# Optimization experiments

Measured on AMD Instinct MI355X. Metric: run time of the kernel, lower is better.

Reference implementation:

```python
import jax, jax.numpy as jnp
import numpy as np

D = 256                      # covariance dim, hardcoded by bottleneck Conv2d(_, 256, 1)
ITER_N = 5                   # SqrtmLayer(output, 5)
_r, _c = np.triu_indices(D)
FLAT_IDX = jnp.asarray(_r * D + _c)   # upper-tri (incl. diag) indices into flattened d*d


def setup_inputs() -> dict:
    key = jax.random.key(0)
    ks = jax.random.split(key, 5)
    B, C, H, W = 64, 2048, 16, 16
    num_classes = 4
    feats = D * (D + 1) // 2  # 32896
    return {
        "features": jax.random.normal(ks[0], (B, C, H, W), jnp.float32),
        "w_bn": jax.random.normal(ks[1], (D, C), jnp.float32) * 0.02,
        "b_bn": jnp.zeros((D,), jnp.float32),
        "w_type": jax.random.normal(ks[2], (num_classes, feats), jnp.float32) * 0.01,
        "b_type": jnp.zeros((num_classes,), jnp.float32),
        "w_flag": jax.random.normal(ks[3], (1, feats), jnp.float32) * 0.01,
        "b_flag": jnp.zeros((1,), jnp.float32),
    }


def _covpool(x):
    # x: [B, d, h, w] -> second-order pooling: x_f @ I_hat @ x_f^T, equivalent
    # to (1/M) * centered @ centered^T  (I_hat = -1/M^2 * ones + 1/M * eye)
    B, d, h, w = x.shape
    M = h * w
    xf = x.reshape(B, d, M)
    centered = xf - xf.mean(axis=2, keepdims=True)
    return jnp.einsum('bim,bjm->bij', centered, centered) / M  # [B, d, d]


def _sqrtm_ns(A, iter_n=ITER_N):
    # Newton-Schulz iteration for matrix square root (iSQRT-COV style)
    B, d, _ = A.shape
    I3 = 3.0 * jnp.eye(d, dtype=A.dtype)
    normA = jnp.trace(A, axis1=1, axis2=2)          # [B], pre-normalization
    An = A / normA[:, None, None]
    ZY = 0.5 * (I3 - An)
    Y = jnp.matmul(An, ZY)
    Z = ZY
    for _ in range(iter_n - 2):
        ZY = 0.5 * (I3 - jnp.matmul(Z, Y))
        Y = jnp.matmul(Y, ZY)
        Z = jnp.matmul(ZY, Z)
    YZY = 0.5 * jnp.matmul(Y, I3 - jnp.matmul(Z, Y))
    return YZY * jnp.sqrt(normA)[:, None, None]     # post-compensation


def reference(features, w_bn, b_bn, w_type, b_type, w_flag, b_flag):
    # 1x1 bottleneck conv: [B, C, H, W] -> [B, 256, H, W]
    x = jnp.einsum('bchw,oc->bohw', features, w_bn) + b_bn[None, :, None, None]
    cov = _covpool(x)                # [B, 256, 256]
    s = _sqrtm_ns(cov)               # [B, 256, 256]
    B = s.shape[0]
    vec = s.reshape(B, D * D)[:, FLAT_IDX]   # triu-vec: [B, 32896]
    type_logits = vec @ w_type.T + b_type    # [B, num_classes]
    flag_logits = vec @ w_flag.T + b_flag    # [B, 1]
    return (type_logits, flag_logits)
```

## Files before the change

kernel.cpp:

```cpp
#include <hip/hip_runtime.h>
#include <math.h>


typedef __attribute__((ext_vector_type(8))) short bf16x8;
typedef __attribute__((ext_vector_type(4))) float f32x4;
typedef __attribute__((ext_vector_type(4))) unsigned u32x4;
typedef __attribute__((ext_vector_type(2))) unsigned u32x2;

__device__ __forceinline__ unsigned fbits(float f) { union { float f; unsigned u; } x; x.f = f; return x.u; }
__device__ __forceinline__ float bitsf(unsigned u) { union { float f; unsigned u; } x; x.u = u; return x.f; }
__device__ __forceinline__ float bf16v(short h) { return bitsf(((unsigned)(unsigned short)h) << 16); }

__device__ __forceinline__ unsigned pack_h(float a, float b) {
  return (fbits(a) >> 16) | (fbits(b) & 0xFFFF0000u);
}
__device__ __forceinline__ unsigned pack_l(float a, float b) {
  float la = a - bitsf(fbits(a) & 0xFFFF0000u);
  float lb = b - bitsf(fbits(b) & 0xFFFF0000u);
  return (fbits(la) >> 16) | (fbits(lb) & 0xFFFF0000u);
}

__device__ __forceinline__ const bf16x8* fragp(const char* M, int kt, int row,
                                               int g, int pl) {
  return (const bf16x8*)(M + (size_t)kt * 32768 + (size_t)row * 128 +
                         ((((pl << 2) + g) ^ (row & 7)) << 4));
}
__device__ __forceinline__ const bf16x8* fragl(const char* L, int kt, int row,
                                               int g, int pl) {
  return (const bf16x8*)(L + kt * 8192 + row * 128 +
                         ((((pl << 2) + g) ^ (row & 7)) << 4));
}

__device__ __forceinline__ void write_quad_g(char* M, int row, int k0,
                                             const float* v) {
  char* rp = M + (size_t)(k0 >> 5) * 32768 + (size_t)row * 128;
  const int s = (k0 & 31) >> 3, bo = (k0 & 7) * 2;
  *(u32x2*)(rp + (((s) ^ (row & 7)) << 4) + bo) =
      (u32x2){pack_h(v[0], v[1]), pack_h(v[2], v[3])};
  *(u32x2*)(rp + (((s + 4) ^ (row & 7)) << 4) + bo) =
      (u32x2){pack_l(v[0], v[1]), pack_l(v[2], v[3])};
}
__device__ __forceinline__ void write_quad_l(char* L, int row, int k0,
                                             const float* v) {
  char* rp = L + (k0 >> 5) * 8192 + row * 128;
  const int s = (k0 & 31) >> 3, bo = (k0 & 7) * 2;
  *(u32x2*)(rp + (((s) ^ (row & 7)) << 4) + bo) =
      (u32x2){pack_h(v[0], v[1]), pack_h(v[2], v[3])};
  *(u32x2*)(rp + (((s + 4) ^ (row & 7)) << 4) + bo) =
      (u32x2){pack_l(v[0], v[1]), pack_l(v[2], v[3])};
}
__device__ __forceinline__ void read_quad_g(const char* M, int row, int k0,
                                            float* v) {
  const char* rp = M + (size_t)(k0 >> 5) * 32768 + (size_t)row * 128;
  const int s = (k0 & 31) >> 3, bo = (k0 & 7) * 2;
  const u32x2 hq = *(const u32x2*)(rp + (((s) ^ (row & 7)) << 4) + bo);
  const u32x2 lq = *(const u32x2*)(rp + (((s + 4) ^ (row & 7)) << 4) + bo);
  v[0] = bitsf(hq[0] << 16) + bitsf(lq[0] << 16);
  v[1] = bitsf(hq[0] & 0xFFFF0000u) + bitsf(lq[0] & 0xFFFF0000u);
  v[2] = bitsf(hq[1] << 16) + bitsf(lq[1] << 16);
  v[3] = bitsf(hq[1] & 0xFFFF0000u) + bitsf(lq[1] & 0xFFFF0000u);
}

#define MFMA3(c, aH, aL, bH, bL)                                            \
  c = __builtin_amdgcn_mfma_f32_16x16x32_bf16(aL, bH, c, 0, 0, 0);          \
  c = __builtin_amdgcn_mfma_f32_16x16x32_bf16(aH, bL, c, 0, 0, 0);          \
  c = __builtin_amdgcn_mfma_f32_16x16x32_bf16(aH, bH, c, 0, 0, 0);

#define LGKM_BAR() do { asm volatile("s_waitcnt lgkmcnt(0)" ::: "memory"); \
                        __builtin_amdgcn_s_barrier(); } while (0)

__global__ __launch_bounds__(256) void prep_k(
    const float* __restrict__ w_bn, const float* __restrict__ w_type,
    const float* __restrict__ w_flag, char* __restrict__ Wf,
    float* __restrict__ W2)
{
  const int bid = blockIdx.x;
  if (bid < 64) {
    const int kt = bid, r = threadIdx.x;
    const float* src = w_bn + (size_t)r * 2048 + kt * 32;
    char* rp = Wf + (size_t)kt * 32768 + (size_t)r * 128;
#pragma unroll
    for (int s = 0; s < 4; ++s) {
      float x[8];
#pragma unroll
      for (int e = 0; e < 8; ++e) x[e] = src[s * 8 + e];
      *(u32x4*)(rp + ((s ^ (r & 7)) << 4)) =
          (u32x4){pack_h(x[0], x[1]), pack_h(x[2], x[3]),
                  pack_h(x[4], x[5]), pack_h(x[6], x[7])};
      *(u32x4*)(rp + (((s + 4) ^ (r & 7)) << 4)) =
          (u32x4){pack_l(x[0], x[1]), pack_l(x[2], x[3]),
                  pack_l(x[4], x[5]), pack_l(x[6], x[7])};
    }
  } else {
    const int idx = bid - 64;
    const int v = idx >> 6, chunk = idx & 63;
    const float* src = (v < 4) ? (w_type + (size_t)v * 32896) : w_flag;
    const int e0 = chunk * 1024 + threadIdx.x * 4;
#pragma unroll
    for (int q = 0; q < 4; ++q) {
      const int e = e0 + q;
      const int i = e >> 8, j = e & 255;
      const int r = i < j ? i : j, c = i < j ? j : i;
      const int t = r * 256 - (r * (r - 1)) / 2 + (c - r);
      W2[(size_t)v * 65536 + e] = src[t] * (i == j ? 1.0f : 0.5f);
    }
  }
}

__global__ __launch_bounds__(512) void conv4_k(
    const char* __restrict__ Wf, const float* __restrict__ F,
    char* __restrict__ X, const float* __restrict__ bias)
{
  __shared__ __align__(16) float bf32[2][64 * 36];
  __shared__ __align__(16) char bfmt[2][8192];

  const int tid = threadIdx.x, lane = tid & 63, w = tid >> 6;
  const int wr = w >> 1, wc = w & 1, fr = lane & 15, g = lane >> 4;
  const int jb = blockIdx.x * 64, bz = blockIdx.y;
  const float* Fb = F + (size_t)bz * 524288;

  const int blc = tid >> 4, blpx = (tid & 15) * 4;
  const int pkpx = tid >> 3, pkq = tid & 3, pkpl = (tid >> 2) & 1;

  f32x4 acc[4][2] = {};
  bf16x8 pa0[4][2], pa1[4][2];
  float4 bl0, bl1;

  auto bload = [&](int t, float4& r) {
    r = *(const float4*)(Fb + ((size_t)t * 32 + blc) * 256 + jb + blpx);
  };
  auto bf32w = [&](int buf, const float4& r) {
    float* p = &bf32[buf][0];
    p[(blpx + 0) * 36 + blc] = r.x;
    p[(blpx + 1) * 36 + blc] = r.y;
    p[(blpx + 2) * 36 + blc] = r.z;
    p[(blpx + 3) * 36 + blc] = r.w;
  };
  auto aload = [&](int t, bf16x8 (*pa)[2]) {
#pragma unroll
    for (int m = 0; m < 4; ++m) {
      const int r = wr * 64 + m * 16 + fr;
#pragma unroll
      for (int pl = 0; pl < 2; ++pl) pa[m][pl] = *fragp(Wf, t, r, g, pl);
    }
  };
  auto pack = [&](int buf) {
    const float* p = &bf32[buf][pkpx * 36 + pkq * 8];
    const f32x4 a = *(const f32x4*)(p);
    const f32x4 b = *(const f32x4*)(p + 4);
    u32x4 outv;
    if (pkpl == 0)
      outv = (u32x4){pack_h(a[0], a[1]), pack_h(a[2], a[3]),
                     pack_h(b[0], b[1]), pack_h(b[2], b[3])};
    else
      outv = (u32x4){pack_l(a[0], a[1]), pack_l(a[2], a[3]),
                     pack_l(b[0], b[1]), pack_l(b[2], b[3])};
    const int slot = ((pkpl << 2) + pkq) ^ (pkpx & 7);
    *(u32x4*)(&bfmt[buf][pkpx * 128 + slot * 16]) = outv;
  };
  auto gemmstep = [&](int buf, bf16x8 (*pa)[2]) {
    bf16x8 bH[2], bL[2];
#pragma unroll
    for (int n = 0; n < 2; ++n) {
      const int r = wc * 32 + n * 16 + fr;
      const char* rp = &bfmt[buf][r * 128];
      bH[n] = *(const bf16x8*)(rp + ((g ^ (r & 7)) << 4));
      bL[n] = *(const bf16x8*)(rp + (((g + 4) ^ (r & 7)) << 4));
    }
#pragma unroll
    for (int m = 0; m < 4; ++m)
#pragma unroll
      for (int n = 0; n < 2; ++n) {
        f32x4 c = acc[m][n];
        MFMA3(c, pa[m][0], pa[m][1], bH[n], bL[n]);
        acc[m][n] = c;
      }
  };

  bload(0, bl0);
  bf32w(0, bl0);
  bload(1, bl1);
  aload(0, pa0);
  LGKM_BAR();
  bf32w(1, bl1);
  pack(0);
  aload(1, pa1);
  bload(2, bl0);
  LGKM_BAR();

  for (int t2 = 0; t2 < 64; t2 += 2) {
    gemmstep(0, pa0);
    if (t2 + 1 < 64) pack(1);
    if (t2 + 2 < 64) { bf32w(0, bl0); aload(t2 + 2, pa0); }
    if (t2 + 3 < 64) bload(t2 + 3, bl1);
    LGKM_BAR();
    gemmstep(1, pa1);
    if (t2 + 2 < 64) pack(0);
    if (t2 + 3 < 64) { bf32w(1, bl1); aload(t2 + 3, pa1); }
    if (t2 + 4 < 64) bload(t2 + 4, bl0);
    LGKM_BAR();
  }

  char* Xb = X + (size_t)bz * 262144;
#pragma unroll
  for (int m = 0; m < 4; ++m) {
    const int gi0 = wr * 64 + m * 16 + g * 4;
#pragma unroll
    for (int n = 0; n < 2; ++n) {
      const int gj = jb + wc * 32 + n * 16 + fr;
      const int ktj = gj >> 5, sj = (gj & 31) >> 3, bo = (gj & 7) * 2;
#pragma unroll
      for (int j = 0; j < 4; ++j) {
        const int gi = gi0 + j;
        char* rp = Xb + (size_t)ktj * 32768 + (size_t)gi * 128;
        const float v = acc[m][n][j] + bias[gi];
        const unsigned u = fbits(v);
        *(short*)(rp + ((sj ^ (gi & 7)) << 4) + bo) = (short)(u >> 16);
        *(short*)(rp + (((sj + 4) ^ (gi & 7)) << 4) + bo) =
            (short)(fbits(v - bitsf(u & 0xFFFF0000u)) >> 16);
      }
    }
  }
}

template <int MODE>
__global__ __launch_bounds__(512) void col_k(
    const char* __restrict__ A1, const char* __restrict__ Bsrc,
    const char* __restrict__ Ys, const char* __restrict__ Zs,
    char* __restrict__ outA, char* __restrict__ outB,
    const float* __restrict__ mu, const float* __restrict__ nrm,
    float* __restrict__ Sf)
{
  __shared__ __align__(16) char Plds[65536];
  const int tid = threadIdx.x, lane = tid & 63, w = tid >> 6;
  const int fr = lane & 15, g = lane >> 4;
  const int blk = blockIdx.x;
  const int bz = (blk & 7) * 8 + ((blk >> 3) & 7);
  const int jb = (blk >> 6) * 64;
  const size_t MB = 262144;
  const char* Ab = A1 + (size_t)bz * MB;
  const char* Bb = Bsrc + (size_t)bz * MB;
  const int r0 = g * 4;

  f32x4 acc[2][4] = {};
  {
    bf16x8 pa[2][2][2], pb[2][4][2];
#pragma unroll
    for (int par = 0; par < 2; ++par) {
#pragma unroll
      for (int m = 0; m < 2; ++m) {
        const int r = w * 32 + m * 16 + fr;
#pragma unroll
        for (int pl = 0; pl < 2; ++pl) pa[par][m][pl] = *fragp(Ab, par, r, g, pl);
      }
#pragma unroll
      for (int n = 0; n < 4; ++n) {
        const int r = jb + n * 16 + fr;
#pragma unroll
        for (int pl = 0; pl < 2; ++pl) pb[par][n][pl] = *fragp(Bb, par, r, g, pl);
      }
    }
    for (int t2 = 0; t2 < 8; t2 += 2) {
#pragma unroll
      for (int par = 0; par < 2; ++par) {
        const int t = t2 + par;
        bf16x8 aH[2], aL[2], bH[4], bL[4];
#pragma unroll
        for (int m = 0; m < 2; ++m) { aH[m] = pa[par][m][0]; aL[m] = pa[par][m][1]; }
#pragma unroll
        for (int n = 0; n < 4; ++n) { bH[n] = pb[par][n][0]; bL[n] = pb[par][n][1]; }
        if (t + 2 < 8) {
#pragma unroll
          for (int m = 0; m < 2; ++m) {
            const int r = w * 32 + m * 16 + fr;
#pragma unroll
            for (int pl = 0; pl < 2; ++pl)
              pa[par][m][pl] = *fragp(Ab, t + 2, r, g, pl);
          }
#pragma unroll
          for (int n = 0; n < 4; ++n) {
            const int r = jb + n * 16 + fr;
#pragma unroll
            for (int pl = 0; pl < 2; ++pl)
              pb[par][n][pl] = *fragp(Bb, t + 2, r, g, pl);
          }
        }
#pragma unroll
        for (int m = 0; m < 2; ++m)
#pragma unroll
          for (int n = 0; n < 4; ++n) {
            f32x4 c = acc[m][n];
            MFMA3(c, aH[m], aL[m], bH[n], bL[n]);
            acc[m][n] = c;
          }
      }
    }
  }

  if constexpr (MODE == 0) {
    const float rn = 1.0f / nrm[bz];
    const float* mub = mu + bz * 256;
    char* oA = outA + (size_t)bz * MB;
    char* oB = outB + (size_t)bz * MB;
#pragma unroll
    for (int m = 0; m < 2; ++m) {
      const int gi0 = w * 32 + m * 16 + r0;
#pragma unroll
      for (int n = 0; n < 4; ++n) {
        const int gj = jb + n * 16 + fr;
        float vv[4], zz[4];
#pragma unroll
        for (int j = 0; j < 4; ++j) {
          const float v =
              (acc[m][n][j] * (1.f / 256.f) - mub[gi0 + j] * mub[gj]) * rn;
          vv[j] = v;
          zz[j] = (gi0 + j == gj ? 1.5f : 0.f) - 0.5f * v;
        }
        write_quad_g(oA, gj, gi0, vv);
        write_quad_g(oB, gj, gi0, zz);
      }
    }
  } else if constexpr (MODE == 1) {
    char* oA = outA + (size_t)bz * MB;
#pragma unroll
    for (int m = 0; m < 2; ++m) {
      const int gi0 = w * 32 + m * 16 + r0;
#pragma unroll
      for (int n = 0; n < 4; ++n) {
        const int gj = jb + n * 16 + fr;
        float av[4], vv[4];
        read_quad_g(Bb, gj, gi0, av);
#pragma unroll
        for (int j = 0; j < 4; ++j) vv[j] = 1.5f * av[j] - 0.5f * acc[m][n][j];
        write_quad_g(oA, gj, gi0, vv);
      }
    }
  } else {
#pragma unroll
    for (int m = 0; m < 2; ++m) {
      const int gi0 = w * 32 + m * 16 + r0;
#pragma unroll
      for (int n = 0; n < 4; ++n) {
        const int jl = n * 16 + fr;
        float vv[4] = {acc[m][n][0], acc[m][n][1], acc[m][n][2], acc[m][n][3]};
        write_quad_l(Plds, jl, gi0, vv);
      }
    }
    const char* Yb = Ys + (size_t)bz * MB;
    const char* Zb = (MODE == 2) ? (Zs + (size_t)bz * MB) : nullptr;
    bf16x8 py[2][2][2], pz[2][2][2];
#pragma unroll
    for (int par = 0; par < 2; ++par)
#pragma unroll
      for (int m = 0; m < 2; ++m) {
        const int r = w * 32 + m * 16 + fr;
#pragma unroll
        for (int pl = 0; pl < 2; ++pl) {
          py[par][m][pl] = *fragp(Yb, par, r, g, pl);
          if constexpr (MODE == 2) pz[par][m][pl] = *fragp(Zb, par, r, g, pl);
        }
      }
    __syncthreads();

    f32x4 aY[2][4] = {}, aZ[2][4] = {};
    for (int t2 = 0; t2 < 8; t2 += 2) {
#pragma unroll
      for (int par = 0; par < 2; ++par) {
        const int t = t2 + par;
        bf16x8 yH[2], yL[2], zH[2], zL[2];
#pragma unroll
        for (int m = 0; m < 2; ++m) {
          yH[m] = py[par][m][0]; yL[m] = py[par][m][1];
          if constexpr (MODE == 2) { zH[m] = pz[par][m][0]; zL[m] = pz[par][m][1]; }
        }
        if (t + 2 < 8) {
#pragma unroll
          for (int m = 0; m < 2; ++m) {
            const int r = w * 32 + m * 16 + fr;
#pragma unroll
            for (int pl = 0; pl < 2; ++pl) {
              py[par][m][pl] = *fragp(Yb, t + 2, r, g, pl);
              if constexpr (MODE == 2) pz[par][m][pl] = *fragp(Zb, t + 2, r, g, pl);
            }
          }
        }
        bf16x8 bH[4], bL[4];
#pragma unroll
        for (int n = 0; n < 4; ++n) {
          const int jl = n * 16 + fr;
          bH[n] = *fragl(Plds, t, jl, g, 0);
          bL[n] = *fragl(Plds, t, jl, g, 1);
        }
#pragma unroll
        for (int m = 0; m < 2; ++m)
#pragma unroll
          for (int n = 0; n < 4; ++n) {
            f32x4 cy = aY[m][n];
            MFMA3(cy, yH[m], yL[m], bH[n], bL[n]);
            aY[m][n] = cy;
            if constexpr (MODE == 2) {
              f32x4 cz = aZ[m][n];
              MFMA3(cz, zH[m], zL[m], bH[n], bL[n]);
              aZ[m][n] = cz;
            }
          }
      }
    }
    if constexpr (MODE == 2) {
      char* oA = outA + (size_t)bz * MB;
      char* oB = outB + (size_t)bz * MB;
#pragma unroll
      for (int m = 0; m < 2; ++m) {
        const int gi0 = w * 32 + m * 16 + r0;
#pragma unroll
        for (int n = 0; n < 4; ++n) {
          const int gj = jb + n * 16 + fr;
          float base[4], vv[4];
          read_quad_g(Yb, gj, gi0, base);
#pragma unroll
          for (int j = 0; j < 4; ++j) vv[j] = 1.5f * base[j] - 0.5f * aY[m][n][j];
          write_quad_g(oA, gj, gi0, vv);
          read_quad_g(Zb, gj, gi0, base);
#pragma unroll
          for (int j = 0; j < 4; ++j) vv[j] = 1.5f * base[j] - 0.5f * aZ[m][n][j];
          write_quad_g(oB, gj, gi0, vv);
        }
      }
    } else {
      const float sq = sqrtf(nrm[bz]);
      float* Sb = Sf + (size_t)bz * 65536;
#pragma unroll
      for (int m = 0; m < 2; ++m) {
        const int gi0 = w * 32 + m * 16 + r0;
#pragma unroll
        for (int n = 0; n < 4; ++n) {
          const int gj = jb + n * 16 + fr;
          float base[4];
          read_quad_g(Yb, gj, gi0, base);
          f32x4 vv;
#pragma unroll
          for (int j = 0; j < 4; ++j)
            vv[j] = (1.5f * base[j] - 0.5f * aY[m][n][j]) * sq;
          *(f32x4*)(Sb + (size_t)gj * 256 + gi0) = vv;
        }
      }
    }
  }
}

__global__ __launch_bounds__(256) void meanvar(const char* __restrict__ X,
                                               float* __restrict__ mu,
                                               float* __restrict__ nrm)
{
  const int b = blockIdx.x, i = threadIdx.x;
  const char* rp0 = X + (size_t)b * 262144 + (size_t)i * 128;
  float s = 0.f, ss = 0.f;
  for (int kt = 0; kt < 8; ++kt) {
    const char* rp = rp0 + kt * 32768;
#pragma unroll
    for (int sl = 0; sl < 4; ++sl) {
      bf16x8 h8 = *(const bf16x8*)(rp + ((sl ^ (i & 7)) << 4));
      bf16x8 l8 = *(const bf16x8*)(rp + (((sl + 4) ^ (i & 7)) << 4));
#pragma unroll
      for (int e = 0; e < 8; ++e) {
        const float v = bf16v(h8[e]) + bf16v(l8[e]);
        s += v; ss += v * v;
      }
    }
  }
  const float m = s * (1.f / 256.f);
  mu[b * 256 + i] = m;
  __shared__ float red[256];
  red[i] = ss * (1.f / 256.f) - m * m;
  __syncthreads();
  for (int o = 128; o > 0; o >>= 1) {
    if (i < o) red[i] += red[i + o];
    __syncthreads();
  }
  if (i == 0) nrm[b] = red[0];
}

__global__ __launch_bounds__(256) void head2(
    const float* __restrict__ Sf, const float* __restrict__ W2,
    const float* __restrict__ b_type, const float* __restrict__ b_flag,
    float* __restrict__ out)
{
  const int b = blockIdx.x, v = blockIdx.y, tid = threadIdx.x;
  const float4* s4 = (const float4*)(Sf + (size_t)b * 65536);
  const float4* w4 = (const float4*)(W2 + (size_t)v * 65536);
  float acc = 0.f;
  for (int i = tid; i < 16384; i += 256) {
    const float4 a = s4[i], c = w4[i];
    acc += a.x * c.x + a.y * c.y + a.z * c.z + a.w * c.w;
  }
  __shared__ float red[256];
  red[tid] = acc;
  __syncthreads();
  for (int o = 128; o > 0; o >>= 1) {
    if (tid < o) red[tid] += red[tid + o];
    __syncthreads();
  }
  if (tid == 0) {
    if (v < 4) out[b * 4 + v] = red[0] + b_type[v];
    else       out[256 + b] = red[0] + b_flag[0];
  }
}

extern "C" void kernel_launch(void* const* d_in, const int* in_sizes, int n_in,
                              void* d_out, int out_size, void* d_ws, size_t ws_size,
                              hipStream_t stream)
{
  const float* features = (const float*)d_in[0];
  const float* w_bn     = (const float*)d_in[1];
  const float* b_bn     = (const float*)d_in[2];
  const float* w_type   = (const float*)d_in[3];
  const float* b_type   = (const float*)d_in[4];
  const float* w_flag   = (const float*)d_in[5];
  const float* b_flag   = (const float*)d_in[6];
  float* out = (float*)d_out;

  char* W = (char*)d_ws;
  const size_t PB = 16777216;
  char* P0 = W;           char* P1 = W + PB;     char* P2 = W + 2 * PB;
  char* P3 = W + 3 * PB;  char* P4 = W + 4 * PB;
  char* Wf = W + 5 * PB;
  float* W2 = (float*)(W + 5 * PB + 2097152);
  float* mu = (float*)(W + 5 * PB + 4194304);
  float* nrm = mu + 64 * 256;
  float* Sf = (float*)P4;

  prep_k<<<dim3(384), dim3(256), 0, stream>>>(w_bn, w_type, w_flag, Wf, W2);
  conv4_k<<<dim3(4, 64), dim3(512), 0, stream>>>(Wf, features, P0, b_bn);
  meanvar<<<dim3(64), dim3(256), 0, stream>>>(P0, mu, nrm);

  const dim3 cg(256), cb(512);
  col_k<0><<<cg, cb, 0, stream>>>(P0, P0, nullptr, nullptr, P1, P2, mu, nrm, nullptr);
  col_k<1><<<cg, cb, 0, stream>>>(P1, P1, nullptr, nullptr, P3, nullptr, nullptr, nullptr, nullptr);
  col_k<2><<<cg, cb, 0, stream>>>(P2, P3, P3, P2, P0, P4, nullptr, nullptr, nullptr);
  col_k<2><<<cg, cb, 0, stream>>>(P4, P0, P0, P4, P1, P2, nullptr, nullptr, nullptr);
  col_k<2><<<cg, cb, 0, stream>>>(P2, P1, P1, P2, P3, P0, nullptr, nullptr, nullptr);
  col_k<3><<<cg, cb, 0, stream>>>(P0, P3, P3, nullptr, nullptr, nullptr, nullptr, nrm, Sf);

  head2<<<dim3(64, 5), dim3(256), 0, stream>>>(Sf, W2, b_type, b_flag, out);
  (void)in_sizes; (void)n_in; (void)out_size; (void)ws_size;
}
```

Measured before the change: 285.4 us.

## Split-K the bottleneck conv and fuse bias, mean and trace into a combine kernel

The 1x1 conv GEMM is split along K into two halves across a new grid dimension, doubling block count from 256 to 512 to better fill the GPU's compute units. A new combine kernel sums the two fp32 partials, adds the bias, writes the split bf16 hi/lo layout, and computes the per-row mean and trace partials, replacing the separate meanvar kernel. It also changes the LDS staging stride from 36 to 33 floats, with scalar reads in the pack step. The cost is extra fp32 partial traffic to global memory, about 64MB written and read back, plus an 8-way partial trace sum in the downstream kernels.

New measurement: 287.1 us. No clear change (+0.6%).

```diff
diff --git a/kernel.cpp b/kernel.cpp
--- a/kernel.cpp
+++ b/kernel.cpp
@@ -107,16 +107,17 @@
   }
 }
 
-__global__ __launch_bounds__(512) void conv4_k(
+__global__ __launch_bounds__(512) void conv5_k(
     const char* __restrict__ Wf, const float* __restrict__ F,
-    char* __restrict__ X, const float* __restrict__ bias)
+    float* __restrict__ Xpart)
 {
-  __shared__ __align__(16) float bf32[2][64 * 36];
+  __shared__ float bf32[2][64 * 33];
   __shared__ __align__(16) char bfmt[2][8192];
 
   const int tid = threadIdx.x, lane = tid & 63, w = tid >> 6;
   const int wr = w >> 1, wc = w & 1, fr = lane & 15, g = lane >> 4;
-  const int jb = blockIdx.x * 64, bz = blockIdx.y;
+  const int jb = blockIdx.x * 64, bz = blockIdx.y, ks = blockIdx.z;
+  const int kb = ks * 32;
   const float* Fb = F + (size_t)bz * 524288;
 
   const int blc = tid >> 4, blpx = (tid & 15) * 4;
@@ -127,34 +128,35 @@
   float4 bl0, bl1;
 
   auto bload = [&](int t, float4& r) {
-    r = *(const float4*)(Fb + ((size_t)t * 32 + blc) * 256 + jb + blpx);
+    r = *(const float4*)(Fb + ((size_t)(kb + t) * 32 + blc) * 256 + jb + blpx);
   };
   auto bf32w = [&](int buf, const float4& r) {
     float* p = &bf32[buf][0];
-    p[(blpx + 0) * 36 + blc] = r.x;
-    p[(blpx + 1) * 36 + blc] = r.y;
-    p[(blpx + 2) * 36 + blc] = r.z;
-    p[(blpx + 3) * 36 + blc] = r.w;
+    p[(blpx + 0) * 33 + blc] = r.x;
+    p[(blpx + 1) * 33 + blc] = r.y;
+    p[(blpx + 2) * 33 + blc] = r.z;
+    p[(blpx + 3) * 33 + blc] = r.w;
   };
   auto aload = [&](int t, bf16x8 (*pa)[2]) {
 #pragma unroll
     for (int m = 0; m < 4; ++m) {
       const int r = wr * 64 + m * 16 + fr;
 #pragma unroll
-      for (int pl = 0; pl < 2; ++pl) pa[m][pl] = *fragp(Wf, t, r, g, pl);
+      for (int pl = 0; pl < 2; ++pl) pa[m][pl] = *fragp(Wf, kb + t, r, g, pl);
     }
   };
   auto pack = [&](int buf) {
-    const float* p = &bf32[buf][pkpx * 36 + pkq * 8];
-    const f32x4 a = *(const f32x4*)(p);
-    const f32x4 b = *(const f32x4*)(p + 4);
+    const float* p = &bf32[buf][pkpx * 33 + pkq * 8];
+    float x[8];
+#pragma unroll
+    for (int e = 0; e < 8; ++e) x[e] = p[e];
     u32x4 outv;
     if (pkpl == 0)
-      outv = (u32x4){pack_h(a[0], a[1]), pack_h(a[2], a[3]),
-                     pack_h(b[0], b[1]), pack_h(b[2], b[3])};
+      outv = (u32x4){pack_h(x[0], x[1]), pack_h(x[2], x[3]),
+                     pack_h(x[4], x[5]), pack_h(x[6], x[7])};
     else
-      outv = (u32x4){pack_l(a[0], a[1]), pack_l(a[2], a[3]),
-                     pack_l(b[0], b[1]), pack_l(b[2], b[3])};
+      outv = (u32x4){pack_l(x[0], x[1]), pack_l(x[2], x[3]),
+                     pack_l(x[4], x[5]), pack_l(x[6], x[7])};
     const int slot = ((pkpl << 2) + pkq) ^ (pkpx & 7);
     *(u32x4*)(&bfmt[buf][pkpx * 128 + slot * 16]) = outv;
   };
@@ -188,39 +190,77 @@
   bload(2, bl0);
   LGKM_BAR();
 
-  for (int t2 = 0; t2 < 64; t2 += 2) {
+  for (int t2 = 0; t2 < 32; t2 += 2) {
     gemmstep(0, pa0);
-    if (t2 + 1 < 64) pack(1);
-    if (t2 + 2 < 64) { bf32w(0, bl0); aload(t2 + 2, pa0); }
-    if (t2 + 3 < 64) bload(t2 + 3, bl1);
+    if (t2 + 1 < 32) pack(1);
+    if (t2 + 2 < 32) { bf32w(0, bl0); aload(t2 + 2, pa0); }
+    if (t2 + 3 < 32) bload(t2 + 3, bl1);
     LGKM_BAR();
     gemmstep(1, pa1);
-    if (t2 + 2 < 64) pack(0);
-    if (t2 + 3 < 64) { bf32w(1, bl1); aload(t2 + 3, pa1); }
-    if (t2 + 4 < 64) bload(t2 + 4, bl0);
+    if (t2 + 2 < 32) pack(0);
+    if (t2 + 3 < 32) { bf32w(1, bl1); aload(t2 + 3, pa1); }
+    if (t2 + 4 < 32) bload(t2 + 4, bl0);
     LGKM_BAR();
   }
 
-  char* Xb = X + (size_t)bz * 262144;
+  float* Xp = Xpart + ((size_t)ks * 64 + bz) * 65536;
 #pragma unroll
   for (int m = 0; m < 4; ++m) {
     const int gi0 = wr * 64 + m * 16 + g * 4;
 #pragma unroll
     for (int n = 0; n < 2; ++n) {
       const int gj = jb + wc * 32 + n * 16 + fr;
-      const int ktj = gj >> 5, sj = (gj & 31) >> 3, bo = (gj & 7) * 2;
-#pragma unroll
-      for (int j = 0; j < 4; ++j) {
-        const int gi = gi0 + j;
-        char* rp = Xb + (size_t)ktj * 32768 + (size_t)gi * 128;
-        const float v = acc[m][n][j] + bias[gi];
-        const unsigned u = fbits(v);
-        *(short*)(rp + ((sj ^ (gi & 7)) << 4) + bo) = (short)(u >> 16);
-        *(short*)(rp + (((sj + 4) ^ (gi & 7)) << 4) + bo) =
-            (short)(fbits(v - bitsf(u & 0xFFFF0000u)) >> 16);
-      }
-    }
-  }
+#pragma unroll
+      for (int j = 0; j < 4; ++j)
+        Xp[(size_t)(gi0 + j) * 256 + gj] = acc[m][n][j];
+    }
+  }
+}
+
+__global__ __launch_bounds__(256) void combine_k(
+    const float* __restrict__ Xp0, const float* __restrict__ Xp1,
+    const float* __restrict__ bias, char* __restrict__ X,
+    float* __restrict__ mu, float* __restrict__ nrm_part)
+{
+  const int chunk = blockIdx.x, bz = blockIdx.y;
+  const int tid = threadIdx.x, lane = tid & 63, w = tid >> 6;
+  const float* p0 = Xp0 + (size_t)bz * 65536;
+  const float* p1 = Xp1 + (size_t)bz * 65536;
+  char* Xb = X + (size_t)bz * 262144;
+  float tracc = 0.f;
+#pragma unroll
+  for (int i = 0; i < 8; ++i) {
+    const int r = chunk * 32 + w * 8 + i;
+    const float4 a = *(const float4*)(p0 + (size_t)r * 256 + lane * 4);
+    const float4 b = *(const float4*)(p1 + (size_t)r * 256 + lane * 4);
+    const float bi = bias[r];
+    float v[4] = {a.x + b.x + bi, a.y + b.y + bi,
+                  a.z + b.z + bi, a.w + b.w + bi};
+    float s = v[0] + v[1] + v[2] + v[3];
+    float ss = v[0] * v[0] + v[1] * v[1] + v[2] * v[2] + v[3] * v[3];
+#pragma unroll
+    for (int o = 32; o > 0; o >>= 1) {
+      s += __shfl_down(s, o);
+      ss += __shfl_down(ss, o);
+    }
+    const float st = __shfl(s, 0), sst = __shfl(ss, 0);
+    const float m = st * (1.f / 256.f);
+    if (lane == 0) mu[bz * 256 + r] = m;
+    tracc += sst * (1.f / 256.f) - m * m;
+    write_quad_g(Xb, r, lane * 4, v);
+  }
+  __shared__ float red[4];
+  if (lane == 0) red[w] = tracc;
+  __syncthreads();
+  if (tid == 0)
+    nrm_part[bz * 8 + chunk] = red[0] + red[1] + red[2] + red[3];
+}
+
+__device__ __forceinline__ float nrm_sum(const float* nrmp, int bz) {
+  float nv = 0.f;
+#pragma unroll
+  for (int q = 0; q < 8; ++q) nv += nrmp[bz * 8 + q];
+  return nv;
 }
 
 template <int MODE>
@@ -228,7 +268,7 @@
     const char* __restrict__ A1, const char* __restrict__ Bsrc,
     const char* __restrict__ Ys, const char* __restrict__ Zs,
     char* __restrict__ outA, char* __restrict__ outB,
-    const float* __restrict__ mu, const float* __restrict__ nrm,
+    const float* __restrict__ mu, const float* __restrict__ nrmp,
     float* __restrict__ Sf)
 {
   __shared__ __align__(16) char Plds[65536];
@@ -298,7 +338,7 @@
   }
 
   if constexpr (MODE == 0) {
-    const float rn = 1.0f / nrm[bz];
+    const float rn = 1.0f / nrm_sum(nrmp, bz);
     const float* mub = mu + bz * 256;
     char* oA = outA + (size_t)bz * MB;
     char* oB = outB + (size_t)bz * MB;
@@ -427,7 +467,7 @@
         }
       }
     } else {
-      const float sq = sqrtf(nrm[bz]);
+      const float sq = sqrtf(nrm_sum(nrmp, bz));
       float* Sb = Sf + (size_t)bz * 65536;
 #pragma unroll
       for (int m = 0; m < 2; ++m) {
@@ -446,38 +486,6 @@
       }
     }
   }
-}
-
-__global__ __launch_bounds__(256) void meanvar(const char* __restrict__ X,
-                                               float* __restrict__ mu,
-                                               float* __restrict__ nrm)
-{
-  const int b = blockIdx.x, i = threadIdx.x;
-  const char* rp0 = X + (size_t)b * 262144 + (size_t)i * 128;
-  float s = 0.f, ss = 0.f;
-  for (int kt = 0; kt < 8; ++kt) {
-    const char* rp = rp0 + kt * 32768;
-#pragma unroll
-    for (int sl = 0; sl < 4; ++sl) {
-      bf16x8 h8 = *(const bf16x8*)(rp + ((sl ^ (i & 7)) << 4));
-      bf16x8 l8 = *(const bf16x8*)(rp + (((sl + 4) ^ (i & 7)) << 4));
-#pragma unroll
-      for (int e = 0; e < 8; ++e) {
-        const float v = bf16v(h8[e]) + bf16v(l8[e]);
-        s += v; ss += v * v;
-      }
-    }
-  }
-  const float m = s * (1.f / 256.f);
-  mu[b * 256 + i] = m;
-  __shared__ float red[256];
-  red[i] = ss * (1.f / 256.f) - m * m;
-  __syncthreads();
-  for (int o = 128; o > 0; o >>= 1) {
-    if (i < o) red[i] += red[i + o];
-    __syncthreads();
-  }
-  if (i == 0) nrm[b] = red[0];
 }
 
 __global__ __launch_bounds__(256) void head2(
@@ -526,20 +534,22 @@
   char* Wf = W + 5 * PB;
   float* W2 = (float*)(W + 5 * PB + 2097152);
   float* mu = (float*)(W + 5 * PB + 4194304);
-  float* nrm = mu + 64 * 256;
+  float* nrm_part = mu + 16384;
+  float* Xpart = (float*)(W + 5 * PB + 8388608);
   float* Sf = (float*)P4;
 
   prep_k<<<dim3(384), dim3(256), 0, stream>>>(w_bn, w_type, w_flag, Wf, W2);
-  conv4_k<<<dim3(4, 64), dim3(512), 0, stream>>>(Wf, features, P0, b_bn);
-  meanvar<<<dim3(64), dim3(256), 0, stream>>>(P0, mu, nrm);
+  conv5_k<<<dim3(4, 64, 2), dim3(512), 0, stream>>>(Wf, features, Xpart);
+  combine_k<<<dim3(8, 64), dim3(256), 0, stream>>>(
+      Xpart, Xpart + 64ull * 65536, b_bn, P0, mu, nrm_part);
 
   const dim3 cg(256), cb(512);
-  col_k<0><<<cg, cb, 0, stream>>>(P0, P0, nullptr, nullptr, P1, P2, mu, nrm, nullptr);
+  col_k<0><<<cg, cb, 0, stream>>>(P0, P0, nullptr, nullptr, P1, P2, mu, nrm_part, nullptr);
   col_k<1><<<cg, cb, 0, stream>>>(P1, P1, nullptr, nullptr, P3, nullptr, nullptr, nullptr, nullptr);
   col_k<2><<<cg, cb, 0, stream>>>(P2, P3, P3, P2, P0, P4, nullptr, nullptr, nullptr);
   col_k<2><<<cg, cb, 0, stream>>>(P4, P0, P0, P4, P1, P2, nullptr, nullptr, nullptr);
   col_k<2><<<cg, cb, 0, stream>>>(P2, P1, P1, P2, P3, P0, nullptr, nullptr, nullptr);
-  col_k<3><<<cg, cb, 0, stream>>>(P0, P3, P3, nullptr, nullptr, nullptr, nullptr, nrm, Sf);
+  col_k<3><<<cg, cb, 0, stream>>>(P0, P3, P3, nullptr, nullptr, nullptr, nullptr, nrm_part, Sf);
 
   head2<<<dim3(64, 5), dim3(256), 0, stream>>>(Sf, W2, b_type, b_flag, out);
   (void)in_sizes; (void)n_in; (void)out_size; (void)ws_size;
```
